# Optimization experiments

Measured on AMD Instinct MI355X. Metric: run time of the kernel, lower is better.

The kernel has to match this reference:

```python
import jax, jax.numpy as jnp
import numpy as np

B, S, D = 8, 2048, 1024

def setup_inputs() -> dict:
    key = jax.random.key(0)
    ks = jax.random.split(key, 7)
    s = 1.0 / np.sqrt(D)
    return {
        "x": jax.random.normal(ks[0], (B, S, D), dtype=jnp.float32),
        "Wq": jax.random.normal(ks[1], (D, D), dtype=jnp.float32) * s,
        "bq": jnp.zeros((D,), dtype=jnp.float32),
        "Wk": jax.random.normal(ks[2], (D, D), dtype=jnp.float32) * s,
        "bk": jnp.zeros((D,), dtype=jnp.float32),
        "Wv": jax.random.normal(ks[3], (D, D), dtype=jnp.float32) * s,
        "bv": jnp.zeros((D,), dtype=jnp.float32),
    }

def reference(x, Wq, bq, Wk, bk, Wv, bv):
    # QKV projections: [B,S,D]
    q = x @ Wq + bq
    k = x @ Wk + bk
    v = x @ Wv + bv
    # scores scaled by sqrt(full input_dim) — single head, per source
    scores = jnp.einsum("bsd,btd->bst", q, k) / jnp.sqrt(jnp.float32(D))
    attn = jax.nn.softmax(scores, axis=2)
    return jnp.einsum("bst,btd->bsd", attn, v)
```

## Files before the change

### kernel.cpp

```cpp
#include <hip/hip_runtime.h>

typedef _Float16 half8 __attribute__((ext_vector_type(8)));
typedef float floatx4 __attribute__((ext_vector_type(4)));

#define AS1 __attribute__((address_space(1)))
#define AS3 __attribute__((address_space(3)))

__global__ __launch_bounds__(256) void wtrans_kernel(
    const float* __restrict__ W0, const float* __restrict__ W1,
    const float* __restrict__ W2, _Float16* __restrict__ Wt)
{
    __shared__ _Float16 t[64 * 72];
    const float* W = (blockIdx.z == 0) ? W0 : (blockIdx.z == 1) ? W1 : W2;
    _Float16* O = Wt + (long)blockIdx.z * 1048576;
    const int tid = threadIdx.x;
    const int kb = blockIdx.y * 64, nb = blockIdx.x * 64;
#pragma unroll
    for (int i = 0; i < 4; i++) {
        int r = (tid >> 4) + i * 16;
        int c = (tid & 15) * 4;
        floatx4 w = *(const floatx4*)&W[(long)(kb + r) * 1024 + nb + c];
#pragma unroll
        for (int j = 0; j < 4; j++) t[(c + j) * 72 + r] = (_Float16)w[j];
    }
    __syncthreads();
    const int c = tid >> 2, rch = (tid & 3) * 16;
    half8 v0 = *(const half8*)&t[c * 72 + rch];
    half8 v1 = *(const half8*)&t[c * 72 + rch + 8];
    _Float16* o = &O[(long)(nb + c) * 1024 + kb + rch];
    *(half8*)o = v0;
    *(half8*)(o + 8) = v1;
}

__global__ __launch_bounds__(256) void f32_to_f16_kernel(
    const float* __restrict__ in, _Float16* __restrict__ out, int n)
{
    for (long i = ((long)blockIdx.x * 256 + threadIdx.x) * 8; i < n;
         i += (long)gridDim.x * 256 * 8) {
        floatx4 a = *(const floatx4*)&in[i];
        floatx4 b = *(const floatx4*)&in[i + 4];
        half8 h;
#pragma unroll
        for (int e = 0; e < 4; e++) { h[e] = (_Float16)a[e]; h[e + 4] = (_Float16)b[e]; }
        *(half8*)&out[i] = h;
    }
}

template <int MODE>
__global__ __launch_bounds__(256) void gemm128_kernel(
    const _Float16* __restrict__ A, const _Float16* __restrict__ Bt,
    void* __restrict__ Cv, const float* __restrict__ bias,
    const float* __restrict__ bias2,
    int nx, int ny,
    int K, int lda, int ldb, int ldc,
    long aBatch, long bBatch, long cBatch, float scale)
{
    constexpr int SMEM_ELEMS = (MODE == 1) ? 17408 : 16384;
    __shared__ _Float16 smem[SMEM_ELEMS];
    _Float16* Ash = smem;
    _Float16* Bsh = smem + 8192;

    const int tid = threadIdx.x;
    const int wave = tid >> 6, lane = tid & 63;
    const int quad = lane >> 4, lr = lane & 15;
    const int wm = wave & 1, wn = wave >> 1;

    const int P = gridDim.x >> 3;
    const int g = (blockIdx.x & 7) * P + (blockIdx.x >> 3);
    const int pplane = nx * ny;
    const int z = g / pplane;
    const int rr = g - z * pplane;
    const int by = rr / nx;
    const int bx = rr - by * nx;
    const int m0 = by * 128, n0 = bx * 128;

    const _Float16* Ab = A + (long)z * aBatch;
    const _Float16* Bb = Bt + (long)z * bBatch;

    const int srow = tid >> 2;
    const int scol = (tid & 3) * 8;
    const long ag0 = (long)(m0 + srow) * lda + scol;
    const long bg0 = (long)(n0 + srow) * ldb + scol;
    const int sdst = tid * 8;

    floatx4 acc[4][4] = {};

    for (int k0 = 0; k0 < K; k0 += 64) {
#pragma unroll
        for (int s = 0; s < 2; s++) {
            const int kk = k0 + s * 32;
            const int so = s * 4096;
            __builtin_amdgcn_global_load_lds(
                (AS1 void*)(Ab + ag0 + kk), (AS3 void*)(Ash + so + sdst), 16, 0, 0);
            __builtin_amdgcn_global_load_lds(
                (AS1 void*)(Ab + ag0 + (long)64 * lda + kk), (AS3 void*)(Ash + so + sdst + 2048), 16, 0, 0);
            __builtin_amdgcn_global_load_lds(
                (AS1 void*)(Bb + bg0 + kk), (AS3 void*)(Bsh + so + sdst), 16, 0, 0);
            __builtin_amdgcn_global_load_lds(
                (AS1 void*)(Bb + bg0 + (long)64 * ldb + kk), (AS3 void*)(Bsh + so + sdst + 2048), 16, 0, 0);
        }
        __syncthreads();

#pragma unroll
        for (int s = 0; s < 2; s++) {
            const int so = s * 4096;
            half8 aF[4], bF[4];
#pragma unroll
            for (int i = 0; i < 4; i++) {
                aF[i] = *(const half8*)&Ash[so + (wm * 64 + i * 16 + lr) * 32 + quad * 8];
                bF[i] = *(const half8*)&Bsh[so + (wn * 64 + i * 16 + lr) * 32 + quad * 8];
            }
#pragma unroll
            for (int mi = 0; mi < 4; mi++)
#pragma unroll
                for (int ni = 0; ni < 4; ni++)
                    acc[mi][ni] = __builtin_amdgcn_mfma_f32_16x16x32_f16(
                        aF[mi], bF[ni], acc[mi][ni], 0, 0, 0);
        }
        __syncthreads();
    }

    if constexpr (MODE == 0) {
        _Float16* C = (_Float16*)Cv + (long)z * cBatch;
        const float* bz = (z == 0 || !bias2) ? bias : bias2;
#pragma unroll
        for (int ni = 0; ni < 4; ni++) {
            const int n = n0 + wn * 64 + ni * 16 + lr;
            const float bv_ = bz ? bz[n] : 0.0f;
#pragma unroll
            for (int mi = 0; mi < 4; mi++) {
                const int mb = m0 + wm * 64 + mi * 16 + quad * 4;
#pragma unroll
                for (int r = 0; r < 4; r++)
                    C[(long)(mb + r) * ldc + n] = (_Float16)((acc[mi][ni][r] + bv_) * scale);
            }
        }
    } else if constexpr (MODE == 1) {
        _Float16* ctile = smem;
#pragma unroll
        for (int ni = 0; ni < 4; ni++) {
            const int nl = wn * 64 + ni * 16 + lr;
            const float bv_ = bias ? bias[n0 + nl] : 0.0f;
#pragma unroll
            for (int mi = 0; mi < 4; mi++) {
                const int ml = wm * 64 + mi * 16 + quad * 4;
#pragma unroll
                for (int r = 0; r < 4; r++)
                    ctile[nl * 136 + ml + r] = (_Float16)((acc[mi][ni][r] + bv_) * scale);
            }
        }
        __syncthreads();
        _Float16* C = (_Float16*)Cv + (long)(m0 >> 11) * cBatch;
        const int t0 = m0 & 2047;
#pragma unroll
        for (int p = 0; p < 8; p++) {
            const int row = p * 16 + (tid >> 4);
            const int seg = (tid & 15) * 8;
            half8 v = *(const half8*)&ctile[row * 136 + seg];
            *(half8*)&C[(long)(n0 + row) * ldc + t0 + seg] = v;
        }
    } else {
        float* C = (float*)Cv + (long)z * cBatch;
#pragma unroll
        for (int ni = 0; ni < 4; ni++) {
            const int n = n0 + wn * 64 + ni * 16 + lr;
#pragma unroll
            for (int mi = 0; mi < 4; mi++) {
                const int mb = m0 + wm * 64 + mi * 16 + quad * 4;
#pragma unroll
                for (int r = 0; r < 4; r++)
                    C[(long)(mb + r) * ldc + n] = acc[mi][ni][r] * scale;
            }
        }
    }
}

#define STAGE_A(d, h, kt) do { \
    __builtin_amdgcn_global_load_lds((AS1 void*)(Ap + (long)((h) * 64) * lda + (long)(kt) * 64), \
        (AS3 void*)(Ash + (d) * 16384 + (h) * 8192 + sdst), 16, 0, 0); \
    __builtin_amdgcn_global_load_lds((AS1 void*)(Ap + (long)((h) * 64 + 128) * lda + (long)(kt) * 64), \
        (AS3 void*)(Ash + (d) * 16384 + (h) * 8192 + 4096 + sdst), 16, 0, 0); \
} while (0)

#define STAGE_B(d, h, kt) do { \
    __builtin_amdgcn_global_load_lds((AS1 void*)(Bp0 + (long)((h) * 32) * ldb + (long)(kt) * 64), \
        (AS3 void*)(Bsh + (d) * 16384 + (h) * 8192 + sdst), 16, 0, 0); \
    __builtin_amdgcn_global_load_lds((AS1 void*)(Bp1 + (long)((h) * 32) * ldb + (long)(kt) * 64), \
        (AS3 void*)(Bsh + (d) * 16384 + (h) * 8192 + 4096 + sdst), 16, 0, 0); \
} while (0)

#define LDA_FRAGS(d, mh) do { \
    _Pragma("unroll") for (int mi_ = 0; mi_ < 4; mi_++) { \
        const _Float16* p_ = &Ash[(d) * 16384 + (mh) * 8192 + (arow + mi_ * 16) * 64]; \
        aF[mi_][0] = *(const half8*)&p_[kq0]; \
        aF[mi_][1] = *(const half8*)&p_[kq1]; \
    } \
} while (0)

#define LDB_FRAGS(d, nh) do { \
    _Pragma("unroll") for (int ni_ = 0; ni_ < 2; ni_++) { \
        const _Float16* p_ = &Bsh[(d) * 16384 + (nh) * 8192 + (brow + ni_ * 16) * 64]; \
        bF[nh][ni_][0] = *(const half8*)&p_[kq0]; \
        bF[nh][ni_][1] = *(const half8*)&p_[kq1]; \
    } \
} while (0)

#define MFMA16(mh, nh) do { \
    __builtin_amdgcn_s_setprio(1); \
    _Pragma("unroll") for (int mi_ = 0; mi_ < 4; mi_++) \
    _Pragma("unroll") for (int ni_ = 0; ni_ < 2; ni_++) { \
        acc[(mh) * 4 + mi_][(nh) * 2 + ni_] = __builtin_amdgcn_mfma_f32_16x16x32_f16( \
            aF[mi_][0], bF[nh][ni_][0], acc[(mh) * 4 + mi_][(nh) * 2 + ni_], 0, 0, 0); \
        acc[(mh) * 4 + mi_][(nh) * 2 + ni_] = __builtin_amdgcn_mfma_f32_16x16x32_f16( \
            aF[mi_][1], bF[nh][ni_][1], acc[(mh) * 4 + mi_][(nh) * 2 + ni_], 0, 0, 0); \
    } \
    __builtin_amdgcn_s_setprio(0); \
} while (0)

#define BAR() do { \
    asm volatile("" ::: "memory"); \
    __builtin_amdgcn_s_barrier(); \
    asm volatile("" ::: "memory"); \
} while (0)

template <int MODE>
__global__ __launch_bounds__(512, 2) void gemm256_kernel(
    const _Float16* __restrict__ A, const _Float16* __restrict__ Bt,
    void* __restrict__ Cv, const float* __restrict__ bias,
    const float* __restrict__ bias2,
    int nx, int ny, int K, int lda, int ldb, int ldc,
    long aBatch, long bBatch, long cBatch, float scale)
{
    __shared__ _Float16 smem[65536];
    _Float16* Ash = smem;
    _Float16* Bsh = smem + 32768;

    const int tid = threadIdx.x;
    const int wave = tid >> 6, lane = tid & 63;
    const int quad = lane >> 4, lr = lane & 15;
    const int wm = wave >> 2, wn = wave & 3;

    const int P = gridDim.x >> 3;
    const int g = (blockIdx.x & 7) * P + (blockIdx.x >> 3);
    const int pplane = nx * ny;
    const int z = g / pplane;
    const int rr = g - z * pplane;
    const int by = rr / nx;
    const int bx = rr - by * nx;
    const int m0 = by * 256, n0 = bx * 256;

    const _Float16* Ab = A + (long)z * aBatch;
    const _Float16* Bb = Bt + (long)z * bBatch;

    const int sr0 = tid >> 3;
    const int sc0 = (tid & 7) ^ (sr0 & 7);
    const _Float16* Ap = Ab + (long)(m0 + sr0) * lda + sc0 * 8;
    const int bc0 = (sr0 & 31) + ((sr0 >> 5) << 6);
    const int bc1 = (sr0 & 31) + (((sr0 >> 5) + 2) << 6);
    const _Float16* Bp0 = Bb + (long)(n0 + bc0) * ldb + sc0 * 8;
    const _Float16* Bp1 = Bb + (long)(n0 + bc1) * ldb + sc0 * 8;
    const int sdst = tid * 8;

    const int kq0 = (quad * 8) ^ ((lr & 7) << 3);
    const int kq1 = (32 + quad * 8) ^ ((lr & 7) << 3);
    const int arow = wm * 64 + lr;
    const int brow = wn * 32 + lr;

    half8 aF[4][2];
    half8 bF[2][2][2];
    floatx4 acc[8][4] = {};
    const int NT = K >> 6;

    STAGE_A(0, 0, 0); STAGE_A(0, 1, 0); STAGE_B(0, 0, 0); STAGE_B(0, 1, 0);
    if (NT > 1) {
        STAGE_A(1, 0, 1); STAGE_B(1, 0, 1);
        asm volatile("s_waitcnt vmcnt(4)" ::: "memory");
    } else {
        asm volatile("s_waitcnt vmcnt(0)" ::: "memory");
    }
    BAR();

    for (int t = 0; t < NT; t++) {
        const int d = t & 1, dn = d ^ 1;
        LDA_FRAGS(d, 0); LDB_FRAGS(d, 0);
        if (t + 1 < NT) STAGE_A(dn, 1, t + 1);
        BAR();
        MFMA16(0, 0);
        BAR();
        LDB_FRAGS(d, 1);
        if (t + 1 < NT) STAGE_B(dn, 1, t + 1);
        BAR();
        MFMA16(0, 1);
        BAR();
        LDA_FRAGS(d, 1);
        if (t + 2 < NT) STAGE_A(d, 0, t + 2);
        BAR();
        MFMA16(1, 0);
        BAR();
        if (t + 2 < NT) STAGE_B(d, 0, t + 2);
        BAR();
        MFMA16(1, 1);
        if (t + 1 < NT) {
            if (t + 2 < NT) asm volatile("s_waitcnt vmcnt(4)" ::: "memory");
            else            asm volatile("s_waitcnt vmcnt(0)" ::: "memory");
        }
        BAR();
    }

    if constexpr (MODE == 0) {
        _Float16* C = (_Float16*)Cv + (long)z * cBatch;
        const float* bz = (z == 0 || !bias2) ? bias : bias2;
#pragma unroll
        for (int ni = 0; ni < 4; ni++) {
            const int n = n0 + wn * 64 + ni * 16 + lr;
            const float bv_ = bz ? bz[n] : 0.0f;
#pragma unroll
            for (int mi = 0; mi < 8; mi++) {
                const int mb = m0 + wm * 128 + mi * 16 + quad * 4;
#pragma unroll
                for (int r = 0; r < 4; r++)
                    C[(long)(mb + r) * ldc + n] = (_Float16)((acc[mi][ni][r] + bv_) * scale);
            }
        }
    } else {
        float* C = (float*)Cv + (long)z * cBatch;
#pragma unroll
        for (int ni = 0; ni < 4; ni++) {
            const int n = n0 + wn * 64 + ni * 16 + lr;
#pragma unroll
            for (int mi = 0; mi < 8; mi++) {
                const int mb = m0 + wm * 128 + mi * 16 + quad * 4;
#pragma unroll
                for (int r = 0; r < 4; r++)
                    C[(long)(mb + r) * ldc + n] = acc[mi][ni][r] * scale;
            }
        }
    }
}

#undef STAGE_A
#undef STAGE_B
#undef LDA_FRAGS
#undef LDB_FRAGS
#undef MFMA16
#undef BAR

__global__ __launch_bounds__(256) void softmax_kernel(_Float16* __restrict__ buf)
{
    const int lane = threadIdx.x & 63;
    const long row = (long)blockIdx.x * 4 + (threadIdx.x >> 6);
    _Float16* p = buf + row * 2048;

    float f[32];
#pragma unroll
    for (int j = 0; j < 4; j++) {
        half8 v = *(const half8*)&p[lane * 8 + j * 512];
#pragma unroll
        for (int e = 0; e < 8; e++) f[j * 8 + e] = (float)v[e];
    }
    float m = -1e30f;
#pragma unroll
    for (int i = 0; i < 32; i++) m = fmaxf(m, f[i]);
#pragma unroll
    for (int off = 32; off; off >>= 1) m = fmaxf(m, __shfl_xor(m, off, 64));
    float s = 0.0f;
#pragma unroll
    for (int i = 0; i < 32; i++) { f[i] = __expf(f[i] - m); s += f[i]; }
#pragma unroll
    for (int off = 32; off; off >>= 1) s += __shfl_xor(s, off, 64);
    const float inv = 1.0f / s;
#pragma unroll
    for (int j = 0; j < 4; j++) {
        half8 v;
#pragma unroll
        for (int e = 0; e < 8; e++) v[e] = (_Float16)(f[j * 8 + e] * inv);
        *(half8*)&p[lane * 8 + j * 512] = v;
    }
}

extern "C" void kernel_launch(void* const* d_in, const int* in_sizes, int n_in,
                              void* d_out, int out_size, void* d_ws, size_t ws_size,
                              hipStream_t stream)
{
    const float* x  = (const float*)d_in[0];
    const float* Wq = (const float*)d_in[1];
    const float* bq = (const float*)d_in[2];
    const float* Wk = (const float*)d_in[3];
    const float* bk = (const float*)d_in[4];
    const float* Wv = (const float*)d_in[5];
    const float* bv = (const float*)d_in[6];

    if (ws_size < 174063616u) return;

    char* ws = (char*)d_ws;
    _Float16* Q  = (_Float16*)(ws + 0);
    _Float16* Vt = (_Float16*)(ws + 67108864);
    _Float16* Sc = (_Float16*)(ws + 100663296);
    _Float16* Wt = (_Float16*)(ws + 167772160);
    _Float16* xb = Sc;
    _Float16* Kb = Q + 16777216;
    float* out = (float*)d_out;

    wtrans_kernel<<<dim3(16, 16, 3), 256, 0, stream>>>(Wq, Wk, Wv, Wt);
    f32_to_f16_kernel<<<2048, 256, 0, stream>>>(x, xb, 16777216);

    gemm256_kernel<0><<<512, 512, 0, stream>>>(
        xb, Wt, Q, bq, bk, 4, 64, 1024, 1024, 1024, 1024,
        0, 1048576, 16777216, 1.0f);
    gemm128_kernel<1><<<1024, 256, 0, stream>>>(
        xb, Wt + 2097152, Vt, bv, nullptr, 8, 128, 1024, 1024, 1024, 2048,
        0, 0, 2097152, 1.0f);

    gemm256_kernel<0><<<512, 512, 0, stream>>>(
        Q, Kb, Sc, nullptr, nullptr, 8, 8, 1024, 1024, 1024, 2048,
        2097152, 2097152, 4194304, 0.03125f);

    softmax_kernel<<<4096, 256, 0, stream>>>(Sc);

    gemm256_kernel<2><<<256, 512, 0, stream>>>(
        Sc, Vt, out, nullptr, nullptr, 4, 8, 2048, 2048, 2048, 1024,
        4194304, 2097152, 2097152, 1.0f);
}
```

Before: 445.3 us.

## Restructure GEMM main loop into unrolled two-tile pipeline with fine-grained vmcnt barriers

Rewrites the 256-tile GEMM main loop to process two K-tiles per iteration with fixed LDS buffer indices. It replaces the eight barriers per tile with four combined vmcnt-wait-plus-barrier points and reorders the MFMA quadrants (snake order) so fragment reuse spans the boundaries. The aim is to cut barrier count and keep more global loads in flight to overlap memory with MFMA. It assumes NT is even and at least 2, and the hand-tuned vmcnt counts and buffer-reuse ordering are fragile for correctness.

```diff
diff --git a/kernel.cpp b/kernel.cpp
--- a/kernel.cpp
+++ b/kernel.cpp
@@ -217,8 +217,8 @@
     __builtin_amdgcn_s_setprio(0); \
 } while (0)
 
-#define BAR() do { \
-    asm volatile("" ::: "memory"); \
+#define VMBAR(n) do { \
+    asm volatile("s_waitcnt vmcnt(" #n ")" ::: "memory"); \
     __builtin_amdgcn_s_barrier(); \
     asm volatile("" ::: "memory"); \
 } while (0)
@@ -270,41 +270,72 @@
     half8 bF[2][2][2];
     floatx4 acc[8][4] = {};
     const int NT = K >> 6;
-
-    STAGE_A(0, 0, 0); STAGE_A(0, 1, 0); STAGE_B(0, 0, 0); STAGE_B(0, 1, 0);
-    if (NT > 1) {
-        STAGE_A(1, 0, 1); STAGE_B(1, 0, 1);
-        asm volatile("s_waitcnt vmcnt(4)" ::: "memory");
-    } else {
-        asm volatile("s_waitcnt vmcnt(0)" ::: "memory");
-    }
-    BAR();
-
-    for (int t = 0; t < NT; t++) {
-        const int d = t & 1, dn = d ^ 1;
-        LDA_FRAGS(d, 0); LDB_FRAGS(d, 0);
-        if (t + 1 < NT) STAGE_A(dn, 1, t + 1);
-        BAR();
+    const int NI = NT >> 1;
+
+    STAGE_A(0, 0, 0); STAGE_B(0, 0, 0); STAGE_B(0, 1, 0); STAGE_A(0, 1, 0);
+    STAGE_A(1, 0, 1); STAGE_B(1, 0, 1);
+    asm volatile("s_waitcnt vmcnt(4)" ::: "memory");
+    __builtin_amdgcn_s_barrier();
+    asm volatile("" ::: "memory");
+
+    for (int i = 0; i < NI - 1; ++i) {
+        const int t1 = 2 * i + 1, t2 = 2 * i + 2, t3 = 2 * i + 3;
+        LDA_FRAGS(0, 0); LDB_FRAGS(0, 0);
+        STAGE_B(1, 1, t1);
+        VMBAR(8);
         MFMA16(0, 0);
-        BAR();
-        LDB_FRAGS(d, 1);
-        if (t + 1 < NT) STAGE_B(dn, 1, t + 1);
-        BAR();
+        LDB_FRAGS(0, 1);
+        STAGE_A(1, 1, t1);
+        VMBAR(8);
         MFMA16(0, 1);
-        BAR();
-        LDA_FRAGS(d, 1);
-        if (t + 2 < NT) STAGE_A(d, 0, t + 2);
-        BAR();
+        LDA_FRAGS(0, 1);
+        STAGE_A(0, 0, t2);
+        VMBAR(8);
+        MFMA16(1, 1);
+        STAGE_B(0, 0, t2);
+        VMBAR(8);
         MFMA16(1, 0);
-        BAR();
-        if (t + 2 < NT) STAGE_B(d, 0, t + 2);
-        BAR();
+        LDA_FRAGS(1, 0); LDB_FRAGS(1, 0);
+        STAGE_B(0, 1, t2);
+        VMBAR(8);
+        MFMA16(0, 0);
+        LDB_FRAGS(1, 1);
+        STAGE_A(0, 1, t2);
+        VMBAR(8);
+        MFMA16(0, 1);
+        LDA_FRAGS(1, 1);
+        STAGE_A(1, 0, t3);
+        VMBAR(8);
         MFMA16(1, 1);
-        if (t + 1 < NT) {
-            if (t + 2 < NT) asm volatile("s_waitcnt vmcnt(4)" ::: "memory");
-            else            asm volatile("s_waitcnt vmcnt(0)" ::: "memory");
-        }
-        BAR();
+        STAGE_B(1, 0, t3);
+        VMBAR(8);
+        MFMA16(1, 0);
+    }
+
+    {
+        const int tl = NT - 1;
+        LDA_FRAGS(0, 0); LDB_FRAGS(0, 0);
+        STAGE_B(1, 1, tl);
+        VMBAR(8);
+        MFMA16(0, 0);
+        LDB_FRAGS(0, 1);
+        STAGE_A(1, 1, tl);
+        VMBAR(8);
+        MFMA16(0, 1);
+        LDA_FRAGS(0, 1);
+        VMBAR(8);
+        MFMA16(1, 1);
+        VMBAR(4);
+        MFMA16(1, 0);
+        LDA_FRAGS(1, 0); LDB_FRAGS(1, 0);
+        VMBAR(2);
+        MFMA16(0, 0);
+        LDB_FRAGS(1, 1);
+        VMBAR(0);
+        MFMA16(0, 1);
+        LDA_FRAGS(1, 1);
+        MFMA16(1, 1);
+        MFMA16(1, 0);
     }
 
     if constexpr (MODE == 0) {
@@ -343,7 +374,7 @@
 #undef LDA_FRAGS
 #undef LDB_FRAGS
 #undef MFMA16
-#undef BAR
+#undef VMBAR
 
 __global__ __launch_bounds__(256) void softmax_kernel(_Float16* __restrict__ buf)
 {
```

After: 423.5 us. 1.05x faster.
